# Kernel optimization log

Measured on AMD Instinct MI355X. Metric: run time of the kernel, lower is better.

The kernel has to match this reference:

```python
import jax, jax.numpy as jnp
import numpy as np

B, K, S, H = 2, 16, 1024, 256
FFN_RATIO = 1.5
D_IN = 3 * H                      # concat of head/tail/context
D_FF = int(D_IN * FFN_RATIO)      # 1152
NEG_INF = -jnp.inf


def setup_inputs() -> dict:
    key = jax.random.key(0)
    ks = jax.random.split(key, 8)
    cand_span_reps = jax.random.normal(ks[0], (B, K, H), dtype=jnp.float32)
    # spans with start < end, leaving room so many pairs have a 'between' gap
    starts = jax.random.randint(ks[1], (B, K), 0, S - 8)
    widths = jax.random.randint(ks[2], (B, K), 1, 6)
    cand_span_ids = jnp.stack([starts, starts + widths], axis=-1).astype(jnp.int64)
    token_reps = jax.random.normal(ks[3], (B, S, H), dtype=jnp.float32)
    token_masks = jnp.ones((B, S), dtype=bool)
    rel_masks = jnp.ones((B, K * K), dtype=bool)
    # FFNProjectionLayer params: Linear(3H -> D_FF) + ReLU + Dropout(0) + Linear(D_FF -> H)
    W1 = jax.random.normal(ks[4], (D_IN, D_FF), dtype=jnp.float32) / np.sqrt(D_IN)
    b1 = jnp.zeros((D_FF,), dtype=jnp.float32)
    W2 = jax.random.normal(ks[5], (D_FF, H), dtype=jnp.float32) / np.sqrt(D_FF)
    b2 = jnp.zeros((H,), dtype=jnp.float32)
    return dict(cand_span_reps=cand_span_reps, cand_span_ids=cand_span_ids,
                token_reps=token_reps, token_masks=token_masks, rel_masks=rel_masks,
                W1=W1, b1=b1, W2=W2, b2=b2)


def reference(cand_span_reps, cand_span_ids, token_reps, token_masks, rel_masks,
              W1, b1, W2, b2):
    b, k, h = cand_span_reps.shape
    s = token_reps.shape[1]
    head = jnp.broadcast_to(cand_span_reps[:, :, None, :], (b, k, k, h))
    tail = jnp.broadcast_to(cand_span_reps[:, None, :, :], (b, k, k, h))
    hs = cand_span_ids[:, :, 0][:, :, None]   # (b,k,1)
    he = cand_span_ids[:, :, 1][:, :, None]
    ts = cand_span_ids[:, :, 0][:, None, :]   # (b,1,k)
    te = cand_span_ids[:, :, 1][:, None, :]
    min_end = jnp.minimum(he, te)              # (b,k,k)
    max_start = jnp.maximum(hs, ts)
    valid_between = (min_end < max_start) & rel_masks.reshape(b, k, k)
    seq = jnp.arange(s)
    # (b,k,k,s) dynamic-range mask: tokens in [min_end, max_start)
    mask = ((seq[None, None, None, :] >= min_end[..., None]) &
            (seq[None, None, None, :] < max_start[..., None]) &
            valid_between[..., None] &
            token_masks[:, None, None, :])
    # (b,k,k,s,h) masked tensor, max-pool over tokens (matches torch masked_fill+max)
    masked = jnp.where(mask[..., None], token_reps[:, None, None, :, :], NEG_INF)
    ctx = jnp.max(masked, axis=3)
    # replace all-masked (-inf) pairs with 0 to keep outputs finite
    ctx = jnp.where(mask.any(axis=3)[..., None], ctx, 0.0)
    rel = jnp.concatenate([head, tail, ctx], axis=-1)        # (b,k,k,3h)
    hid = jax.nn.relu(rel @ W1 + b1)                          # dropout p=0 -> identity
    out = hid @ W2 + b2                                       # (b,k,k,h)
    return out.reshape(b, k * k, h)
```

## Files before the change

### kernel.cpp

```cpp
#include <hip/hip_runtime.h>
#include <hip/hip_bf16.h>
#include <float.h>

#define BB 2
#define KK 16
#define SS 1024
#define HH 256
#define D_IN 768
#define D_FF 1152
#define NPAIR (BB*KK*KK)

#define CH 16
#define NCH (SS/CH)

typedef __attribute__((ext_vector_type(8))) short short8;
typedef __attribute__((ext_vector_type(4))) float floatx4;

__device__ __forceinline__ unsigned short f2bf(float f) {
    union { float f; unsigned u; } v; v.f = f;
    unsigned r = v.u + 0x7fffu + ((v.u >> 16) & 1u);
    return (unsigned short)(r >> 16);
}
__device__ __forceinline__ float bf2f(unsigned short s) {
    union { unsigned u; float f; } v; v.u = ((unsigned)s) << 16;
    return v.f;
}

__device__ __forceinline__ float rmax_f32(const float* __restrict__ p, int n)
{
    float m0 = -FLT_MAX, m1 = -FLT_MAX, m2 = -FLT_MAX, m3 = -FLT_MAX;
    int t = 0;
    for (; t + 4 <= n; t += 4) {
        float a = p[(size_t)(t + 0) * HH];
        float b = p[(size_t)(t + 1) * HH];
        float c = p[(size_t)(t + 2) * HH];
        float d = p[(size_t)(t + 3) * HH];
        m0 = fmaxf(m0, a); m1 = fmaxf(m1, b);
        m2 = fmaxf(m2, c); m3 = fmaxf(m3, d);
    }
    for (; t < n; ++t) m0 = fmaxf(m0, p[(size_t)t * HH]);
    return fmaxf(fmaxf(m0, m1), fmaxf(m2, m3));
}
__device__ __forceinline__ float rmax_bf16(const unsigned short* __restrict__ p, int n)
{
    float m0 = -FLT_MAX, m1 = -FLT_MAX, m2 = -FLT_MAX, m3 = -FLT_MAX;
    int t = 0;
    for (; t + 4 <= n; t += 4) {
        float a = bf2f(p[(size_t)(t + 0) * HH]);
        float b = bf2f(p[(size_t)(t + 1) * HH]);
        float c = bf2f(p[(size_t)(t + 2) * HH]);
        float d = bf2f(p[(size_t)(t + 3) * HH]);
        m0 = fmaxf(m0, a); m1 = fmaxf(m1, b);
        m2 = fmaxf(m2, c); m3 = fmaxf(m3, d);
    }
    for (; t < n; ++t) m0 = fmaxf(m0, bf2f(p[(size_t)t * HH]));
    return fmaxf(fmaxf(m0, m1), fmaxf(m2, m3));
}

#define W1_TILES (24*36)
#define W2_TILES (36*8)
#define PREP_BLOCKS (W1_TILES + W2_TILES + BB*NCH)
__global__ void prep_kernel(const float* __restrict__ W1, unsigned short* __restrict__ Wt1,
                            const float* __restrict__ W2, unsigned short* __restrict__ Wt2,
                            const float* __restrict__ tok, unsigned short* __restrict__ cmax)
{
    int bid = blockIdx.x;
    if (bid < W1_TILES + W2_TILES) {
        __shared__ unsigned short t[32][33];
        const float* W; unsigned short* Wt; int Kd, Nd, tk, tn;
        if (bid < W1_TILES) { W = W1; Wt = Wt1; Kd = D_IN;  Nd = D_FF; tk = bid / 36; tn = bid % 36; }
        else { bid -= W1_TILES; W = W2; Wt = Wt2; Kd = D_FF; Nd = HH;  tk = bid / 8;  tn = bid % 8; }
        const int r = threadIdx.x >> 5;
        const int c = threadIdx.x & 31;
        #pragma unroll
        for (int rr = r; rr < 32; rr += 8)
            t[rr][c] = f2bf(W[(size_t)(tk * 32 + rr) * Nd + tn * 32 + c]);
        __syncthreads();
        #pragma unroll
        for (int rr = r; rr < 32; rr += 8)
            Wt[(size_t)(tn * 32 + rr) * Kd + tk * 32 + c] = t[c][rr];
    } else {
        bid -= W1_TILES + W2_TILES;
        const int b = bid >> 6;
        const int c = bid & 63;
        const int h = threadIdx.x;
        const float* p = tok + ((size_t)(b * SS + c * CH)) * HH + h;
        float m0 = -FLT_MAX, m1 = -FLT_MAX, m2 = -FLT_MAX, m3 = -FLT_MAX;
        #pragma unroll
        for (int t = 0; t < CH; t += 4) {
            float a  = p[(size_t)(t + 0) * HH];
            float bb = p[(size_t)(t + 1) * HH];
            float cc = p[(size_t)(t + 2) * HH];
            float d  = p[(size_t)(t + 3) * HH];
            m0 = fmaxf(m0, a); m1 = fmaxf(m1, bb);
            m2 = fmaxf(m2, cc); m3 = fmaxf(m3, d);
        }
        cmax[(size_t)(b * NCH + c) * HH + h] = f2bf(fmaxf(fmaxf(m0, m1), fmaxf(m2, m3)));
    }
}

__global__ void build_x_kernel(const float* __restrict__ reps,
                               const int*   __restrict__ ids,
                               const float* __restrict__ tok,
                               const unsigned short* __restrict__ cmax,
                               unsigned short* __restrict__ X)
{
    const int p = blockIdx.x;
    const int h = threadIdx.x;
    const int b = p >> 8;
    const int i = (p >> 4) & 15;
    const int j = p & 15;

    const bool is64 = (ids[1] == 0);
    int hs, he, ts, te;
    if (is64) {
        hs = ids[((b*KK + i)*2 + 0) * 2];
        he = ids[((b*KK + i)*2 + 1) * 2];
        ts = ids[((b*KK + j)*2 + 0) * 2];
        te = ids[((b*KK + j)*2 + 1) * 2];
    } else {
        hs = ids[(b*KK + i)*2 + 0];
        he = ids[(b*KK + i)*2 + 1];
        ts = ids[(b*KK + j)*2 + 0];
        te = ids[(b*KK + j)*2 + 1];
    }

    const int lo = min(he, te);
    const int hi = max(hs, ts);

    const float head = reps[(size_t)(b*KK + i)*HH + h];
    const float tail = reps[(size_t)(b*KK + j)*HH + h];

    float m;
    if (lo < hi) {
        const float* trow = tok  + (size_t)b * SS  * HH + h;
        const unsigned short* crow = cmax + (size_t)b * NCH * HH + h;
        const int csta = (lo + CH - 1) >> 4;
        const int cend = hi >> 4;
        if (csta < cend) {
            float mA = rmax_f32(trow + (size_t)lo * HH, csta * CH - lo);
            float mB = rmax_bf16(crow + (size_t)csta * HH, cend - csta);
            float mC = rmax_f32(trow + (size_t)(cend * CH) * HH, hi - cend * CH);
            m = fmaxf(fmaxf(mA, mB), mC);
        } else {
            m = rmax_f32(trow + (size_t)lo * HH, hi - lo);
        }
    } else {
        m = 0.0f;
    }

    unsigned short* xr = X + (size_t)p * D_IN;
    xr[h]        = f2bf(head);
    xr[HH + h]   = f2bf(tail);
    xr[2*HH + h] = f2bf(m);
}

template<int BKT, int MODE>
__global__ __launch_bounds__(256)
void gemm_bf16_mfma(const unsigned short* __restrict__ A,
                    const unsigned short* __restrict__ Bt,
                    const float* __restrict__ bias,
                    void* __restrict__ Cout,
                    int M, int N, int K, int kPerSplit)
{
    constexpr int LDKT = BKT + 8;
    constexpr int NSEG = BKT / 32;
    __shared__ unsigned short As[64 * LDKT];
    __shared__ unsigned short Bs[64 * LDKT];

    const int tid  = threadIdx.x;
    const int lane = tid & 63;
    const int wave = tid >> 6;
    const int wm   = wave & 1;
    const int wn   = wave >> 1;
    const int quad = lane >> 4;
    const int l16  = lane & 15;

    const int rowBase = blockIdx.y * 64;
    const int colBase = blockIdx.x * 64;
    const int kbeg = blockIdx.z * kPerSplit;
    const int kend = kbeg + kPerSplit;

    int srow[NSEG], scol[NSEG];
    #pragma unroll
    for (int s = 0; s < NSEG; ++s) {
        const int lin = tid * NSEG + s;
        srow[s] = lin / (BKT / 8);
        scol[s] = (lin % (BKT / 8)) * 8;
    }

    floatx4 acc00 = {0.f,0.f,0.f,0.f}, acc01 = acc00, acc10 = acc00, acc11 = acc00;

    short8 pa[NSEG], pb[NSEG];
    #pragma unroll
    for (int s = 0; s < NSEG; ++s) {
        pa[s] = *(const short8*)&A [(size_t)(rowBase + srow[s]) * K + kbeg + scol[s]];
        pb[s] = *(const short8*)&Bt[(size_t)(colBase + srow[s]) * K + kbeg + scol[s]];
    }

    for (int k0 = kbeg; k0 < kend; k0 += BKT) {
        #pragma unroll
        for (int s = 0; s < NSEG; ++s) {
            *(short8*)&As[srow[s] * LDKT + scol[s]] = pa[s];
            *(short8*)&Bs[srow[s] * LDKT + scol[s]] = pb[s];
        }
        __syncthreads();

        const int kn = k0 + BKT;
        if (kn < kend) {
            #pragma unroll
            for (int s = 0; s < NSEG; ++s) {
                pa[s] = *(const short8*)&A [(size_t)(rowBase + srow[s]) * K + kn + scol[s]];
                pb[s] = *(const short8*)&Bt[(size_t)(colBase + srow[s]) * K + kn + scol[s]];
            }
        }

        #pragma unroll
        for (int kk = 0; kk < NSEG; ++kk) {
            const int ko = kk * 32 + quad * 8;
            short8 a0 = *(const short8*)&As[(wm * 32      + l16) * LDKT + ko];
            short8 a1 = *(const short8*)&As[(wm * 32 + 16 + l16) * LDKT + ko];
            short8 b0 = *(const short8*)&Bs[(wn * 32      + l16) * LDKT + ko];
            short8 b1 = *(const short8*)&Bs[(wn * 32 + 16 + l16) * LDKT + ko];
            acc00 = __builtin_amdgcn_mfma_f32_16x16x32_bf16(a0, b0, acc00, 0, 0, 0);
            acc01 = __builtin_amdgcn_mfma_f32_16x16x32_bf16(a0, b1, acc01, 0, 0, 0);
            acc10 = __builtin_amdgcn_mfma_f32_16x16x32_bf16(a1, b0, acc10, 0, 0, 0);
            acc11 = __builtin_amdgcn_mfma_f32_16x16x32_bf16(a1, b1, acc11, 0, 0, 0);
        }
        __syncthreads();
    }

    floatx4 accs[2][2] = {{acc00, acc01}, {acc10, acc11}};
    #pragma unroll
    for (int mt = 0; mt < 2; ++mt) {
        #pragma unroll
        for (int nt = 0; nt < 2; ++nt) {
            #pragma unroll
            for (int r = 0; r < 4; ++r) {
                const int m = rowBase + wm * 32 + mt * 16 + quad * 4 + r;
                const int n = colBase + wn * 32 + nt * 16 + l16;
                float v = accs[mt][nt][r];
                if (MODE == 1) {
                    v = fmaxf(v + bias[n], 0.0f);
                    ((unsigned short*)Cout)[(size_t)m * N + n] = f2bf(v);
                } else {
                    ((float*)Cout)[(size_t)blockIdx.z * M * N + (size_t)m * N + n] = v;
                }
            }
        }
    }
}

__global__ void reduce_bias_act(const float* __restrict__ P,
                                const float* __restrict__ bias,
                                float* __restrict__ out,
                                int MN, int N, int splits)
{
    const int i4 = blockIdx.x * blockDim.x + threadIdx.x;
    if (i4 * 4 >= MN) return;
    float4 s = *(const float4*)(P + (size_t)i4 * 4);
    for (int z = 1; z < splits; ++z) {
        float4 q = *(const float4*)(P + (size_t)z * MN + (size_t)i4 * 4);
        s.x += q.x; s.y += q.y; s.z += q.z; s.w += q.w;
    }
    const int n = (i4 * 4) % N;
    const float4 bv = *(const float4*)(bias + n);
    s.x += bv.x; s.y += bv.y; s.z += bv.z; s.w += bv.w;
    *(float4*)(out + (size_t)i4 * 4) = s;
}

extern "C" void kernel_launch(void* const* d_in, const int* in_sizes, int n_in,
                              void* d_out, int out_size, void* d_ws, size_t ws_size,
                              hipStream_t stream)
{
    const float* reps = (const float*)d_in[0];
    const int*   ids  = (const int*)  d_in[1];
    const float* tok  = (const float*)d_in[2];
    const float* W1   = (const float*)d_in[5];
    const float* b1   = (const float*)d_in[6];
    const float* W2   = (const float*)d_in[7];
    const float* b2   = (const float*)d_in[8];
    float* out = (float*)d_out;

    char* wsb = (char*)d_ws;
    unsigned short* Wt1  = (unsigned short*)(wsb);
    unsigned short* Wt2  = (unsigned short*)(wsb + 1769472);
    unsigned short* cmax = (unsigned short*)(wsb + 2359296);
    unsigned short* X    = (unsigned short*)(wsb + 2424832);
    unsigned short* hid  = (unsigned short*)(wsb + 3211264);
    float*          P2   = (float*)         (wsb + 4390912);

    const size_t MN2 = (size_t)NPAIR * HH;
    const int S2 = 4;

    prep_kernel<<<PREP_BLOCKS, 256, 0, stream>>>(W1, Wt1, W2, Wt2, tok, cmax);

    build_x_kernel<<<NPAIR, HH, 0, stream>>>(reps, ids, tok, cmax, X);

    gemm_bf16_mfma<64, 1><<<dim3(D_FF / 64, NPAIR / 64, 1), 256, 0, stream>>>(
        X, Wt1, b1, hid, NPAIR, D_FF, D_IN, D_IN);

    gemm_bf16_mfma<32, 0><<<dim3(HH / 64, NPAIR / 64, S2), 256, 0, stream>>>(
        hid, Wt2, nullptr, P2, NPAIR, HH, D_FF, D_FF / S2);

    reduce_bias_act<<<(int)(MN2 / 4 + 255) / 256, 256, 0, stream>>>(
        P2, b2, out, (int)MN2, HH, S2);
}
```

Baseline: 98.32 us.

## Fuse context-pooling into prep kernel and drop split-K reduction for second GEMM

The context max-pool is merged into the weight-transpose prep launch, with one wave per pair reading float4 tokens directly instead of using chunk-max precomputation. The second GEMM switches from 4-way split-K plus a separate reduce kernel to 32x32 tiles with bias fused into the output write. The aim is to cut launches from five to three and remove the partial-sum round trip. In exchange, long spans scan every token instead of chunk maxima, and the second GEMM gets smaller tiles with a longer K loop per block.

```diff
diff --git a/kernel.cpp b/kernel.cpp
--- a/kernel.cpp
+++ b/kernel.cpp
@@ -10,10 +10,8 @@
 #define D_FF 1152
 #define NPAIR (BB*KK*KK)
 
-#define CH 16
-#define NCH (SS/CH)
-
 typedef __attribute__((ext_vector_type(8))) short short8;
+typedef __attribute__((ext_vector_type(4))) short short4v;
 typedef __attribute__((ext_vector_type(4))) float floatx4;
 
 __device__ __forceinline__ unsigned short f2bf(float f) {
@@ -21,48 +19,31 @@
     unsigned r = v.u + 0x7fffu + ((v.u >> 16) & 1u);
     return (unsigned short)(r >> 16);
 }
-__device__ __forceinline__ float bf2f(unsigned short s) {
-    union { unsigned u; float f; } v; v.u = ((unsigned)s) << 16;
-    return v.f;
-}
-
-__device__ __forceinline__ float rmax_f32(const float* __restrict__ p, int n)
-{
-    float m0 = -FLT_MAX, m1 = -FLT_MAX, m2 = -FLT_MAX, m3 = -FLT_MAX;
-    int t = 0;
-    for (; t + 4 <= n; t += 4) {
-        float a = p[(size_t)(t + 0) * HH];
-        float b = p[(size_t)(t + 1) * HH];
-        float c = p[(size_t)(t + 2) * HH];
-        float d = p[(size_t)(t + 3) * HH];
-        m0 = fmaxf(m0, a); m1 = fmaxf(m1, b);
-        m2 = fmaxf(m2, c); m3 = fmaxf(m3, d);
-    }
-    for (; t < n; ++t) m0 = fmaxf(m0, p[(size_t)t * HH]);
-    return fmaxf(fmaxf(m0, m1), fmaxf(m2, m3));
-}
-__device__ __forceinline__ float rmax_bf16(const unsigned short* __restrict__ p, int n)
-{
-    float m0 = -FLT_MAX, m1 = -FLT_MAX, m2 = -FLT_MAX, m3 = -FLT_MAX;
-    int t = 0;
-    for (; t + 4 <= n; t += 4) {
-        float a = bf2f(p[(size_t)(t + 0) * HH]);
-        float b = bf2f(p[(size_t)(t + 1) * HH]);
-        float c = bf2f(p[(size_t)(t + 2) * HH]);
-        float d = bf2f(p[(size_t)(t + 3) * HH]);
-        m0 = fmaxf(m0, a); m1 = fmaxf(m1, b);
-        m2 = fmaxf(m2, c); m3 = fmaxf(m3, d);
-    }
-    for (; t < n; ++t) m0 = fmaxf(m0, bf2f(p[(size_t)t * HH]));
-    return fmaxf(fmaxf(m0, m1), fmaxf(m2, m3));
+__device__ __forceinline__ float4 fmax4(float4 a, float4 b) {
+    float4 r;
+    r.x = fmaxf(a.x, b.x); r.y = fmaxf(a.y, b.y);
+    r.z = fmaxf(a.z, b.z); r.w = fmaxf(a.w, b.w);
+    return r;
+}
+__device__ __forceinline__ void store4bf(unsigned short* dst, float4 v) {
+    short4v u;
+    u.x = (short)f2bf(v.x); u.y = (short)f2bf(v.y);
+    u.z = (short)f2bf(v.z); u.w = (short)f2bf(v.w);
+    *(short4v*)dst = u;
 }
 
 #define W1_TILES (24*36)
 #define W2_TILES (36*8)
-#define PREP_BLOCKS (W1_TILES + W2_TILES + BB*NCH)
-__global__ void prep_kernel(const float* __restrict__ W1, unsigned short* __restrict__ Wt1,
-                            const float* __restrict__ W2, unsigned short* __restrict__ Wt2,
-                            const float* __restrict__ tok, unsigned short* __restrict__ cmax)
+#define BX_BLOCKS (NPAIR/4)
+#define PREP_BLOCKS (W1_TILES + W2_TILES + BX_BLOCKS)
+
+__global__ __launch_bounds__(256)
+void prep_build_kernel(const float* __restrict__ W1, unsigned short* __restrict__ Wt1,
+                       const float* __restrict__ W2, unsigned short* __restrict__ Wt2,
+                       const float* __restrict__ tok,
+                       const float* __restrict__ reps,
+                       const int*   __restrict__ ids,
+                       unsigned short* __restrict__ X)
 {
     int bid = blockIdx.x;
     if (bid < W1_TILES + W2_TILES) {
@@ -79,37 +60,17 @@
         #pragma unroll
         for (int rr = r; rr < 32; rr += 8)
             Wt[(size_t)(tn * 32 + rr) * Kd + tk * 32 + c] = t[c][rr];
-    } else {
-        bid -= W1_TILES + W2_TILES;
-        const int b = bid >> 6;
-        const int c = bid & 63;
-        const int h = threadIdx.x;
-        const float* p = tok + ((size_t)(b * SS + c * CH)) * HH + h;
-        float m0 = -FLT_MAX, m1 = -FLT_MAX, m2 = -FLT_MAX, m3 = -FLT_MAX;
-        #pragma unroll
-        for (int t = 0; t < CH; t += 4) {
-            float a  = p[(size_t)(t + 0) * HH];
-            float bb = p[(size_t)(t + 1) * HH];
-            float cc = p[(size_t)(t + 2) * HH];
-            float d  = p[(size_t)(t + 3) * HH];
-            m0 = fmaxf(m0, a); m1 = fmaxf(m1, bb);
-            m2 = fmaxf(m2, cc); m3 = fmaxf(m3, d);
-        }
-        cmax[(size_t)(b * NCH + c) * HH + h] = f2bf(fmaxf(fmaxf(m0, m1), fmaxf(m2, m3)));
-    }
-}
-
-__global__ void build_x_kernel(const float* __restrict__ reps,
-                               const int*   __restrict__ ids,
-                               const float* __restrict__ tok,
-                               const unsigned short* __restrict__ cmax,
-                               unsigned short* __restrict__ X)
-{
-    const int p = blockIdx.x;
-    const int h = threadIdx.x;
+        return;
+    }
+
+    bid -= (W1_TILES + W2_TILES);
+    const int wave = threadIdx.x >> 6;
+    const int lane = threadIdx.x & 63;
+    const int p = bid * 4 + wave;
     const int b = p >> 8;
     const int i = (p >> 4) & 15;
     const int j = p & 15;
+    const int h4 = lane * 4;
 
     const bool is64 = (ids[1] == 0);
     int hs, he, ts, te;
@@ -124,47 +85,49 @@
         ts = ids[(b*KK + j)*2 + 0];
         te = ids[(b*KK + j)*2 + 1];
     }
-
     const int lo = min(he, te);
     const int hi = max(hs, ts);
 
-    const float head = reps[(size_t)(b*KK + i)*HH + h];
-    const float tail = reps[(size_t)(b*KK + j)*HH + h];
-
-    float m;
+    const float4 head = *(const float4*)(reps + (size_t)(b*KK + i) * HH + h4);
+    const float4 tail = *(const float4*)(reps + (size_t)(b*KK + j) * HH + h4);
+
+    float4 m;
     if (lo < hi) {
-        const float* trow = tok  + (size_t)b * SS  * HH + h;
-        const unsigned short* crow = cmax + (size_t)b * NCH * HH + h;
-        const int csta = (lo + CH - 1) >> 4;
-        const int cend = hi >> 4;
-        if (csta < cend) {
-            float mA = rmax_f32(trow + (size_t)lo * HH, csta * CH - lo);
-            float mB = rmax_bf16(crow + (size_t)csta * HH, cend - csta);
-            float mC = rmax_f32(trow + (size_t)(cend * CH) * HH, hi - cend * CH);
-            m = fmaxf(fmaxf(mA, mB), mC);
-        } else {
-            m = rmax_f32(trow + (size_t)lo * HH, hi - lo);
-        }
+        const float* base = tok + (size_t)b * SS * HH + h4;
+        float4 a[8];
+        #pragma unroll
+        for (int s = 0; s < 8; ++s) a[s] = make_float4(-FLT_MAX,-FLT_MAX,-FLT_MAX,-FLT_MAX);
+        int t = lo;
+        for (; t + 8 <= hi; t += 8) {
+            #pragma unroll
+            for (int s = 0; s < 8; ++s) {
+                float4 v = *(const float4*)(base + (size_t)(t + s) * HH);
+                a[s] = fmax4(a[s], v);
+            }
+        }
+        for (; t < hi; ++t)
+            a[0] = fmax4(a[0], *(const float4*)(base + (size_t)t * HH));
+        a[0] = fmax4(a[0], a[1]); a[2] = fmax4(a[2], a[3]);
+        a[4] = fmax4(a[4], a[5]); a[6] = fmax4(a[6], a[7]);
+        a[0] = fmax4(a[0], a[2]); a[4] = fmax4(a[4], a[6]);
+        m = fmax4(a[0], a[4]);
     } else {
-        m = 0.0f;
+        m = make_float4(0.f, 0.f, 0.f, 0.f);
     }
 
     unsigned short* xr = X + (size_t)p * D_IN;
-    xr[h]        = f2bf(head);
-    xr[HH + h]   = f2bf(tail);
-    xr[2*HH + h] = f2bf(m);
-}
-
-template<int BKT, int MODE>
+    store4bf(xr + h4,          head);
+    store4bf(xr + HH + h4,     tail);
+    store4bf(xr + 2*HH + h4,   m);
+}
+
 __global__ __launch_bounds__(256)
-void gemm_bf16_mfma(const unsigned short* __restrict__ A,
-                    const unsigned short* __restrict__ Bt,
-                    const float* __restrict__ bias,
-                    void* __restrict__ Cout,
-                    int M, int N, int K, int kPerSplit)
-{
-    constexpr int LDKT = BKT + 8;
-    constexpr int NSEG = BKT / 32;
+void gemm1_kernel(const unsigned short* __restrict__ A,
+                  const unsigned short* __restrict__ Bt,
+                  const float* __restrict__ bias,
+                  unsigned short* __restrict__ C)
+{
+    constexpr int K = D_IN, N = D_FF, BK = 64, LDKT = BK + 8;
     __shared__ unsigned short As[64 * LDKT];
     __shared__ unsigned short Bs[64 * LDKT];
 
@@ -178,45 +141,43 @@
 
     const int rowBase = blockIdx.y * 64;
     const int colBase = blockIdx.x * 64;
-    const int kbeg = blockIdx.z * kPerSplit;
-    const int kend = kbeg + kPerSplit;
-
-    int srow[NSEG], scol[NSEG];
-    #pragma unroll
-    for (int s = 0; s < NSEG; ++s) {
-        const int lin = tid * NSEG + s;
-        srow[s] = lin / (BKT / 8);
-        scol[s] = (lin % (BKT / 8)) * 8;
+
+    int srow[2], scol[2];
+    #pragma unroll
+    for (int s = 0; s < 2; ++s) {
+        const int lin = tid * 2 + s;
+        srow[s] = lin >> 3;
+        scol[s] = (lin & 7) * 8;
     }
 
     floatx4 acc00 = {0.f,0.f,0.f,0.f}, acc01 = acc00, acc10 = acc00, acc11 = acc00;
 
-    short8 pa[NSEG], pb[NSEG];
-    #pragma unroll
-    for (int s = 0; s < NSEG; ++s) {
-        pa[s] = *(const short8*)&A [(size_t)(rowBase + srow[s]) * K + kbeg + scol[s]];
-        pb[s] = *(const short8*)&Bt[(size_t)(colBase + srow[s]) * K + kbeg + scol[s]];
-    }
-
-    for (int k0 = kbeg; k0 < kend; k0 += BKT) {
-        #pragma unroll
-        for (int s = 0; s < NSEG; ++s) {
+    short8 pa[2], pb[2];
+    #pragma unroll
+    for (int s = 0; s < 2; ++s) {
+        pa[s] = *(const short8*)&A [(size_t)(rowBase + srow[s]) * K + scol[s]];
+        pb[s] = *(const short8*)&Bt[(size_t)(colBase + srow[s]) * K + scol[s]];
+    }
+
+    for (int k0 = 0; k0 < K; k0 += BK) {
+        #pragma unroll
+        for (int s = 0; s < 2; ++s) {
             *(short8*)&As[srow[s] * LDKT + scol[s]] = pa[s];
             *(short8*)&Bs[srow[s] * LDKT + scol[s]] = pb[s];
         }
         __syncthreads();
 
-        const int kn = k0 + BKT;
-        if (kn < kend) {
+        const int kn = k0 + BK;
+        if (kn < K) {
             #pragma unroll
-            for (int s = 0; s < NSEG; ++s) {
+            for (int s = 0; s < 2; ++s) {
                 pa[s] = *(const short8*)&A [(size_t)(rowBase + srow[s]) * K + kn + scol[s]];
                 pb[s] = *(const short8*)&Bt[(size_t)(colBase + srow[s]) * K + kn + scol[s]];
             }
         }
 
         #pragma unroll
-        for (int kk = 0; kk < NSEG; ++kk) {
+        for (int kk = 0; kk < 2; ++kk) {
             const int ko = kk * 32 + quad * 8;
             short8 a0 = *(const short8*)&As[(wm * 32      + l16) * LDKT + ko];
             short8 a1 = *(const short8*)&As[(wm * 32 + 16 + l16) * LDKT + ko];
@@ -232,41 +193,74 @@
 
     floatx4 accs[2][2] = {{acc00, acc01}, {acc10, acc11}};
     #pragma unroll
-    for (int mt = 0; mt < 2; ++mt) {
-        #pragma unroll
-        for (int nt = 0; nt < 2; ++nt) {
+    for (int mt = 0; mt < 2; ++mt)
+        #pragma unroll
+        for (int nt = 0; nt < 2; ++nt)
             #pragma unroll
             for (int r = 0; r < 4; ++r) {
                 const int m = rowBase + wm * 32 + mt * 16 + quad * 4 + r;
                 const int n = colBase + wn * 32 + nt * 16 + l16;
-                float v = accs[mt][nt][r];
-                if (MODE == 1) {
-                    v = fmaxf(v + bias[n], 0.0f);
-                    ((unsigned short*)Cout)[(size_t)m * N + n] = f2bf(v);
-                } else {
-                    ((float*)Cout)[(size_t)blockIdx.z * M * N + (size_t)m * N + n] = v;
-                }
+                float v = fmaxf(accs[mt][nt][r] + bias[n], 0.0f);
+                C[(size_t)m * N + n] = f2bf(v);
             }
-        }
-    }
-}
-
-__global__ void reduce_bias_act(const float* __restrict__ P,
-                                const float* __restrict__ bias,
-                                float* __restrict__ out,
-                                int MN, int N, int splits)
-{
-    const int i4 = blockIdx.x * blockDim.x + threadIdx.x;
-    if (i4 * 4 >= MN) return;
-    float4 s = *(const float4*)(P + (size_t)i4 * 4);
-    for (int z = 1; z < splits; ++z) {
-        float4 q = *(const float4*)(P + (size_t)z * MN + (size_t)i4 * 4);
-        s.x += q.x; s.y += q.y; s.z += q.z; s.w += q.w;
-    }
-    const int n = (i4 * 4) % N;
-    const float4 bv = *(const float4*)(bias + n);
-    s.x += bv.x; s.y += bv.y; s.z += bv.z; s.w += bv.w;
-    *(float4*)(out + (size_t)i4 * 4) = s;
+}
+
+__global__ __launch_bounds__(256)
+void gemm2_kernel(const unsigned short* __restrict__ A,
+                  const unsigned short* __restrict__ Bt,
+                  const float* __restrict__ bias,
+                  float* __restrict__ C)
+{
+    constexpr int K = D_FF, N = HH, BK = 64, LDKT = BK + 8;
+    __shared__ unsigned short As[32 * LDKT];
+    __shared__ unsigned short Bs[32 * LDKT];
+
+    const int tid  = threadIdx.x;
+    const int lane = tid & 63;
+    const int wave = tid >> 6;
+    const int wm   = wave & 1;
+    const int wn   = wave >> 1;
+    const int quad = lane >> 4;
+    const int l16  = lane & 15;
+
+    const int rowBase = blockIdx.y * 32;
+    const int colBase = blockIdx.x * 32;
+
+    const int srow = tid >> 3;
+    const int scol = (tid & 7) * 8;
+
+    floatx4 acc = {0.f,0.f,0.f,0.f};
+
+    short8 pa = *(const short8*)&A [(size_t)(rowBase + srow) * K + scol];
+    short8 pb = *(const short8*)&Bt[(size_t)(colBase + srow) * K + scol];
+
+    for (int k0 = 0; k0 < K; k0 += BK) {
+        *(short8*)&As[srow * LDKT + scol] = pa;
+        *(short8*)&Bs[srow * LDKT + scol] = pb;
+        __syncthreads();
+
+        const int kn = k0 + BK;
+        if (kn < K) {
+            pa = *(const short8*)&A [(size_t)(rowBase + srow) * K + kn + scol];
+            pb = *(const short8*)&Bt[(size_t)(colBase + srow) * K + kn + scol];
+        }
+
+        #pragma unroll
+        for (int kk = 0; kk < 2; ++kk) {
+            const int ko = kk * 32 + quad * 8;
+            short8 a = *(const short8*)&As[(wm * 16 + l16) * LDKT + ko];
+            short8 b = *(const short8*)&Bs[(wn * 16 + l16) * LDKT + ko];
+            acc = __builtin_amdgcn_mfma_f32_16x16x32_bf16(a, b, acc, 0, 0, 0);
+        }
+        __syncthreads();
+    }
+
+    #pragma unroll
+    for (int r = 0; r < 4; ++r) {
+        const int m = rowBase + wm * 16 + quad * 4 + r;
+        const int n = colBase + wn * 16 + l16;
+        C[(size_t)m * N + n] = acc[r] + bias[n];
+    }
 }
 
 extern "C" void kernel_launch(void* const* d_in, const int* in_sizes, int n_in,
@@ -283,26 +277,15 @@
     float* out = (float*)d_out;
 
     char* wsb = (char*)d_ws;
-    unsigned short* Wt1  = (unsigned short*)(wsb);
-    unsigned short* Wt2  = (unsigned short*)(wsb + 1769472);
-    unsigned short* cmax = (unsigned short*)(wsb + 2359296);
-    unsigned short* X    = (unsigned short*)(wsb + 2424832);
-    unsigned short* hid  = (unsigned short*)(wsb + 3211264);
-    float*          P2   = (float*)         (wsb + 4390912);
-
-    const size_t MN2 = (size_t)NPAIR * HH;
-    const int S2 = 4;
-
-    prep_kernel<<<PREP_BLOCKS, 256, 0, stream>>>(W1, Wt1, W2, Wt2, tok, cmax);
-
-    build_x_kernel<<<NPAIR, HH, 0, stream>>>(reps, ids, tok, cmax, X);
-
-    gemm_bf16_mfma<64, 1><<<dim3(D_FF / 64, NPAIR / 64, 1), 256, 0, stream>>>(
-        X, Wt1, b1, hid, NPAIR, D_FF, D_IN, D_IN);
-
-    gemm_bf16_mfma<32, 0><<<dim3(HH / 64, NPAIR / 64, S2), 256, 0, stream>>>(
-        hid, Wt2, nullptr, P2, NPAIR, HH, D_FF, D_FF / S2);
-
-    reduce_bias_act<<<(int)(MN2 / 4 + 255) / 256, 256, 0, stream>>>(
-        P2, b2, out, (int)MN2, HH, S2);
-}
+    unsigned short* Wt1 = (unsigned short*)(wsb);
+    unsigned short* Wt2 = (unsigned short*)(wsb + 1769472);
+    unsigned short* X   = (unsigned short*)(wsb + 2359296);
+    unsigned short* hid = (unsigned short*)(wsb + 3145728);
+
+    prep_build_kernel<<<PREP_BLOCKS, 256, 0, stream>>>(W1, Wt1, W2, Wt2,
+                                                       tok, reps, ids, X);
+
+    gemm1_kernel<<<dim3(D_FF / 64, NPAIR / 64), 256, 0, stream>>>(X, Wt1, b1, hid);
+
+    gemm2_kernel<<<dim3(HH / 32, NPAIR / 32), 256, 0, stream>>>(hid, Wt2, b2, out);
+}
```

Result: slower. 140.1 us (+42.5%).

## Replace split-K second GEMM with 32x32-tile kernel writing output directly

Applied to the files above, without the earlier changes.

The second GEMM drops its 4-way split-K with fp32 partials and the separate reduce/bias kernel. It now uses 32x32 output tiles over the full K with the bias fused, so one launch writes the final output. This removes a kernel launch and the partial-sum round trip through memory. In exchange each block loops over all of K=1152 with only one MFMA accumulator per wave, which lowers per-wave arithmetic intensity. The first GEMM is simply specialized from the template with no change in behavior.

```diff
diff --git a/kernel.cpp b/kernel.cpp
--- a/kernel.cpp
+++ b/kernel.cpp
@@ -155,16 +155,13 @@
     xr[2*HH + h] = f2bf(m);
 }
 
-template<int BKT, int MODE>
 __global__ __launch_bounds__(256)
-void gemm_bf16_mfma(const unsigned short* __restrict__ A,
-                    const unsigned short* __restrict__ Bt,
-                    const float* __restrict__ bias,
-                    void* __restrict__ Cout,
-                    int M, int N, int K, int kPerSplit)
-{
-    constexpr int LDKT = BKT + 8;
-    constexpr int NSEG = BKT / 32;
+void gemm1_kernel(const unsigned short* __restrict__ A,
+                  const unsigned short* __restrict__ Bt,
+                  const float* __restrict__ bias,
+                  unsigned short* __restrict__ C)
+{
+    constexpr int K = D_IN, N = D_FF, BK = 64, LDKT = BK + 8;
     __shared__ unsigned short As[64 * LDKT];
     __shared__ unsigned short Bs[64 * LDKT];
 
@@ -178,45 +175,43 @@
 
     const int rowBase = blockIdx.y * 64;
     const int colBase = blockIdx.x * 64;
-    const int kbeg = blockIdx.z * kPerSplit;
-    const int kend = kbeg + kPerSplit;
-
-    int srow[NSEG], scol[NSEG];
+
+    int srow[2], scol[2];
     #pragma unroll
-    for (int s = 0; s < NSEG; ++s) {
-        const int lin = tid * NSEG + s;
-        srow[s] = lin / (BKT / 8);
-        scol[s] = (lin % (BKT / 8)) * 8;
+    for (int s = 0; s < 2; ++s) {
+        const int lin = tid * 2 + s;
+        srow[s] = lin >> 3;
+        scol[s] = (lin & 7) * 8;
     }
 
     floatx4 acc00 = {0.f,0.f,0.f,0.f}, acc01 = acc00, acc10 = acc00, acc11 = acc00;
 
-    short8 pa[NSEG], pb[NSEG];
+    short8 pa[2], pb[2];
     #pragma unroll
-    for (int s = 0; s < NSEG; ++s) {
-        pa[s] = *(const short8*)&A [(size_t)(rowBase + srow[s]) * K + kbeg + scol[s]];
-        pb[s] = *(const short8*)&Bt[(size_t)(colBase + srow[s]) * K + kbeg + scol[s]];
-    }
-
-    for (int k0 = kbeg; k0 < kend; k0 += BKT) {
-        #pragma unroll
-        for (int s = 0; s < NSEG; ++s) {
+    for (int s = 0; s < 2; ++s) {
+        pa[s] = *(const short8*)&A [(size_t)(rowBase + srow[s]) * K + scol[s]];
+        pb[s] = *(const short8*)&Bt[(size_t)(colBase + srow[s]) * K + scol[s]];
+    }
+
+    for (int k0 = 0; k0 < K; k0 += BK) {
+        #pragma unroll
+        for (int s = 0; s < 2; ++s) {
             *(short8*)&As[srow[s] * LDKT + scol[s]] = pa[s];
             *(short8*)&Bs[srow[s] * LDKT + scol[s]] = pb[s];
         }
         __syncthreads();
 
-        const int kn = k0 + BKT;
-        if (kn < kend) {
+        const int kn = k0 + BK;
+        if (kn < K) {
             #pragma unroll
-            for (int s = 0; s < NSEG; ++s) {
+            for (int s = 0; s < 2; ++s) {
                 pa[s] = *(const short8*)&A [(size_t)(rowBase + srow[s]) * K + kn + scol[s]];
                 pb[s] = *(const short8*)&Bt[(size_t)(colBase + srow[s]) * K + kn + scol[s]];
             }
         }
 
         #pragma unroll
-        for (int kk = 0; kk < NSEG; ++kk) {
+        for (int kk = 0; kk < 2; ++kk) {
             const int ko = kk * 32 + quad * 8;
             short8 a0 = *(const short8*)&As[(wm * 32      + l16) * LDKT + ko];
             short8 a1 = *(const short8*)&As[(wm * 32 + 16 + l16) * LDKT + ko];
@@ -232,41 +227,74 @@
 
     floatx4 accs[2][2] = {{acc00, acc01}, {acc10, acc11}};
     #pragma unroll
-    for (int mt = 0; mt < 2; ++mt) {
-        #pragma unroll
-        for (int nt = 0; nt < 2; ++nt) {
+    for (int mt = 0; mt < 2; ++mt)
+        #pragma unroll
+        for (int nt = 0; nt < 2; ++nt)
             #pragma unroll
             for (int r = 0; r < 4; ++r) {
                 const int m = rowBase + wm * 32 + mt * 16 + quad * 4 + r;
                 const int n = colBase + wn * 32 + nt * 16 + l16;
-                float v = accs[mt][nt][r];
-                if (MODE == 1) {
-                    v = fmaxf(v + bias[n], 0.0f);
-                    ((unsigned short*)Cout)[(size_t)m * N + n] = f2bf(v);
-                } else {
-                    ((float*)Cout)[(size_t)blockIdx.z * M * N + (size_t)m * N + n] = v;
-                }
+                float v = fmaxf(accs[mt][nt][r] + bias[n], 0.0f);
+                C[(size_t)m * N + n] = f2bf(v);
             }
-        }
-    }
-}
-
-__global__ void reduce_bias_act(const float* __restrict__ P,
-                                const float* __restrict__ bias,
-                                float* __restrict__ out,
-                                int MN, int N, int splits)
-{
-    const int i4 = blockIdx.x * blockDim.x + threadIdx.x;
-    if (i4 * 4 >= MN) return;
-    float4 s = *(const float4*)(P + (size_t)i4 * 4);
-    for (int z = 1; z < splits; ++z) {
-        float4 q = *(const float4*)(P + (size_t)z * MN + (size_t)i4 * 4);
-        s.x += q.x; s.y += q.y; s.z += q.z; s.w += q.w;
-    }
-    const int n = (i4 * 4) % N;
-    const float4 bv = *(const float4*)(bias + n);
-    s.x += bv.x; s.y += bv.y; s.z += bv.z; s.w += bv.w;
-    *(float4*)(out + (size_t)i4 * 4) = s;
+}
+
+__global__ __launch_bounds__(256)
+void gemm2_kernel(const unsigned short* __restrict__ A,
+                  const unsigned short* __restrict__ Bt,
+                  const float* __restrict__ bias,
+                  float* __restrict__ C)
+{
+    constexpr int K = D_FF, N = HH, BK = 64, LDKT = BK + 8;
+    __shared__ unsigned short As[32 * LDKT];
+    __shared__ unsigned short Bs[32 * LDKT];
+
+    const int tid  = threadIdx.x;
+    const int lane = tid & 63;
+    const int wave = tid >> 6;
+    const int wm   = wave & 1;
+    const int wn   = wave >> 1;
+    const int quad = lane >> 4;
+    const int l16  = lane & 15;
+
+    const int rowBase = blockIdx.y * 32;
+    const int colBase = blockIdx.x * 32;
+
+    const int srow = tid >> 3;
+    const int scol = (tid & 7) * 8;
+
+    floatx4 acc = {0.f,0.f,0.f,0.f};
+
+    short8 pa = *(const short8*)&A [(size_t)(rowBase + srow) * K + scol];
+    short8 pb = *(const short8*)&Bt[(size_t)(colBase + srow) * K + scol];
+
+    for (int k0 = 0; k0 < K; k0 += BK) {
+        *(short8*)&As[srow * LDKT + scol] = pa;
+        *(short8*)&Bs[srow * LDKT + scol] = pb;
+        __syncthreads();
+
+        const int kn = k0 + BK;
+        if (kn < K) {
+            pa = *(const short8*)&A [(size_t)(rowBase + srow) * K + kn + scol];
+            pb = *(const short8*)&Bt[(size_t)(colBase + srow) * K + kn + scol];
+        }
+
+        #pragma unroll
+        for (int kk = 0; kk < 2; ++kk) {
+            const int ko = kk * 32 + quad * 8;
+            short8 a = *(const short8*)&As[(wm * 16 + l16) * LDKT + ko];
+            short8 b = *(const short8*)&Bs[(wn * 16 + l16) * LDKT + ko];
+            acc = __builtin_amdgcn_mfma_f32_16x16x32_bf16(a, b, acc, 0, 0, 0);
+        }
+        __syncthreads();
+    }
+
+    #pragma unroll
+    for (int r = 0; r < 4; ++r) {
+        const int m = rowBase + wm * 16 + quad * 4 + r;
+        const int n = colBase + wn * 16 + l16;
+        C[(size_t)m * N + n] = acc[r] + bias[n];
+    }
 }
 
 extern "C" void kernel_launch(void* const* d_in, const int* in_sizes, int n_in,
@@ -288,21 +316,12 @@
     unsigned short* cmax = (unsigned short*)(wsb + 2359296);
     unsigned short* X    = (unsigned short*)(wsb + 2424832);
     unsigned short* hid  = (unsigned short*)(wsb + 3211264);
-    float*          P2   = (float*)         (wsb + 4390912);
-
-    const size_t MN2 = (size_t)NPAIR * HH;
-    const int S2 = 4;
 
     prep_kernel<<<PREP_BLOCKS, 256, 0, stream>>>(W1, Wt1, W2, Wt2, tok, cmax);
 
     build_x_kernel<<<NPAIR, HH, 0, stream>>>(reps, ids, tok, cmax, X);
 
-    gemm_bf16_mfma<64, 1><<<dim3(D_FF / 64, NPAIR / 64, 1), 256, 0, stream>>>(
-        X, Wt1, b1, hid, NPAIR, D_FF, D_IN, D_IN);
-
-    gemm_bf16_mfma<32, 0><<<dim3(HH / 64, NPAIR / 64, S2), 256, 0, stream>>>(
-        hid, Wt2, nullptr, P2, NPAIR, HH, D_FF, D_FF / S2);
-
-    reduce_bias_act<<<(int)(MN2 / 4 + 255) / 256, 256, 0, stream>>>(
-        P2, b2, out, (int)MN2, HH, S2);
-}
+    gemm1_kernel<<<dim3(D_FF / 64, NPAIR / 64), 256, 0, stream>>>(X, Wt1, b1, hid);
+
+    gemm2_kernel<<<dim3(HH / 32, NPAIR / 32), 256, 0, stream>>>(hid, Wt2, b2, out);
+}
```

Measured after the change: 100.6 us. 1.02x slower.
